# Kernel tuning notes

Measured on AMD Instinct MI355X. Metric: run time of the kernel, lower is better.

## Reference

```python
import jax, jax.numpy as jnp
import numpy as np

B, D = 32768, 64  # batch, input_dim == output_dim (k == d forced by the layer's nesting)


def setup_inputs() -> dict:
    key = jax.random.key(0)
    ks = jax.random.split(key, 9)
    f = lambda k_, sh, s=1.0: jax.random.normal(k_, sh, dtype=jnp.float32) * s
    # 0.02 / 0.1 scales keep tanh out of full saturation (init choice, not math change)
    return {
        "e1": f(ks[0], (B, D)),
        "p": f(ks[1], (B, D)),
        "e2": f(ks[2], (B, D)),
        "er": f(ks[3], (B, D)),
        "T1": f(ks[4], (D, D, D), 0.02),
        "T2": f(ks[5], (D, D, D), 0.02),
        "T3": f(ks[6], (D, D, D), 0.02),
        "W": f(ks[7], (D, 2 * D), 0.1),
        "b": jnp.zeros((D, 1), dtype=jnp.float32),
    }


def reference(e1, p, e2, er, T1, T2, T3, W, b):
    def ntn(a, c, T):
        # a, c: (B, d); T: (k, d, d) -> (k, B)
        bil = jnp.einsum("bi,kij,bj->kb", a, T, c)          # batched bilinear forms
        ff = jnp.einsum("kf,bf->kb", W, jnp.concatenate([a, c], axis=1))
        return jnp.tanh(bil + ff + b)                        # b: (k,1) broadcasts over batch

    a1 = ntn(e1, p, T1).T   # (B, k)
    c2 = ntn(p, e2, T2).T   # (B, k)  (original recomputes this for ur; identical value)
    u = ntn(a1, c2, T3)     # (k, B)
    ar = ntn(er, p, T1).T   # (B, k)
    ur = ntn(ar, c2, T3)    # (k, B)
    # concat of (B, d, 1) slabs along last axis -> (B, d, 2)
    return jnp.stack([u.T, ur.T], axis=2)
```

## Files before the change

### kernel.cpp

```cpp
#include <hip/hip_runtime.h>
#include <hip/hip_bf16.h>
#include <math.h>

#define BATCH 32768

typedef __attribute__((ext_vector_type(8))) short short8v;
typedef __attribute__((ext_vector_type(4))) float f32x4;
typedef __attribute__((ext_vector_type(2))) float f32x2;
typedef unsigned short u16;
typedef unsigned char u8;

#define MFMA16 __builtin_amdgcn_mfma_f32_16x16x32_bf16

#define TILE_AB 32768
#define TILE_C  65536
#define SMB     81920

#define WS_T(t) ((size_t)(t)*524288)
#define WS_W    1572864

static __device__ __forceinline__ u16 f2bf(float x) {
    __hip_bfloat16 h = __float2bfloat16(x);
    return *reinterpret_cast<u16*>(&h);
}
static __device__ __forceinline__ float bf2f(u16 v) {
    __hip_bfloat16 h = *reinterpret_cast<__hip_bfloat16*>(&v);
    return __bfloat162float(h);
}

__global__ void presplit_kernel(const float* __restrict__ T1, const float* __restrict__ T2,
                                const float* __restrict__ T3, const float* __restrict__ W,
                                u8* __restrict__ ws)
{
    const int idx = blockIdx.x * 256 + threadIdx.x;
    const int NT = 3 * 262144;
    if (idx < NT) {
        const int t = idx >> 18;
        const int r = idx & 262143;
        const int k = r >> 12, i = (r >> 6) & 63, j = r & 63;
        const float* Ts = (t == 0) ? T1 : (t == 1) ? T2 : T3;
        const int kt = k >> 4, klr = k & 15;
        const int pc = (j >> 3) ^ (klr & 7);
        const size_t base = WS_T(t) + (size_t)i * 8192 + kt * 2048 + klr * 128
                          + pc * 16 + (j & 7) * 2;
        *(u16*)(ws + base) = f2bf(Ts[r]);
    } else if (idx < NT + 16384) {
        const int r = idx - NT;
        const int plane = r >> 12, k = (r >> 6) & 63, j = r & 63;
        const int half = plane >> 1, lo = plane & 1;
        const float x = W[k * 128 + half * 64 + j];
        const u16 hh = f2bf(x);
        const u16 v = lo ? f2bf(x - bf2f(hh)) : hh;
        *(u16*)(ws + WS_W + (size_t)plane * 8192 + (k * 64 + j) * 2) = v;
    }
}

__device__ __forceinline__ void stage16(const void* g, void* l) {
    __builtin_amdgcn_global_load_lds((const __attribute__((address_space(1))) unsigned int*)g,
                                     (__attribute__((address_space(3))) unsigned int*)l, 16, 0, 0);
}
__device__ __forceinline__ void stage_slice(u8* sm, const u8* slice, int buf, int w, int l) {
    stage16(slice + w * 1024 + l * 16, sm + buf * 8192 + w * 1024);
}

struct Frag2 { short8v h, l; };
__device__ __forceinline__ Frag2 split8(const float* __restrict__ src) {
    Frag2 f;
#pragma unroll
    for (int e = 0; e < 8; ++e) {
        const float x = src[e];
        const u16 h = f2bf(x);
        f.h[e] = (short)h;
        f.l[e] = (short)f2bf(x - bf2f(h));
    }
    return f;
}
__device__ __forceinline__ Frag2 gather_c(const u8* sm, int b, int f0) {
    float tmp[8];
#pragma unroll
    for (int e = 0; e < 8; ++e)
        tmp[e] = *(const float*)(sm + TILE_C + (f0 + e) * 256 + b * 4);
    return split8(tmp);
}
__device__ __forceinline__ void gather_ab(const u8* sm, int b, int f0, Frag2& fa, Frag2& fb) {
    float t0[8], t1[8];
#pragma unroll
    for (int e = 0; e < 8; ++e) {
        const f32x2 v = *(const f32x2*)(sm + TILE_AB + (size_t)(f0 + e) * 512 + b * 8);
        t0[e] = v.x; t1[e] = v.y;
    }
    fa = split8(t0); fb = split8(t1);
}
__device__ __forceinline__ f32x4 mfma3(short8v Ah, short8v Al, short8v Bh, short8v Bl, f32x4 acc) {
    acc = MFMA16(Ah, Bh, acc, 0, 0, 0);
    acc = MFMA16(Ah, Bl, acc, 0, 0, 0);
    acc = MFMA16(Al, Bh, acc, 0, 0, 0);
    return acc;
}

template<int MODE>
__device__ void pass_run(u8* sm, const u8* __restrict__ ws,
                         const float* __restrict__ gC, const float* __restrict__ gA0,
                         const float* __restrict__ gA1,
                         const float* __restrict__ bias, float* __restrict__ outg,
                         int B0, int w, int kt, int jh, int l, int lr, int lq, int tid)
{
    constexpr int NV = (MODE == 1) ? 1 : 2;
    const u8* tws = ws + WS_T(MODE);

    stage_slice(sm, tws,                    0, w, l);
    stage_slice(sm, tws + (size_t)1 * 8192, 1, w, l);
    stage_slice(sm, tws + (size_t)2 * 8192, 2, w, l);

    short8v Bh[4], Bl[4];
#pragma unroll
    for (int nt = 0; nt < 4; ++nt) {
        const int b = nt * 16 + lr;
        Frag2 f;
        if (MODE < 2) f = split8(gC + (size_t)(B0 + b) * 64 + jh * 32 + lq * 8);
        else          f = gather_c(sm, b, jh * 32 + lq * 8);
        Bh[nt] = f.h; Bl[nt] = f.l;
    }

    f32x4 bil[NV][4];
    {
        const u16* Wp = (const u16*)(ws + WS_W);
        if (jh == 0) {
            short8v w2h[2], w2l[2];
#pragma unroll
            for (int h = 0; h < 2; ++h) {
                const int off = (kt * 16 + lr) * 64 + h * 32 + lq * 8;
                w2h[h] = *(const short8v*)(Wp + 8192 + off);
                w2l[h] = *(const short8v*)(Wp + 12288 + off);
            }
            const f32x4 bv4 = *(const f32x4*)(bias + kt * 16 + lq * 4);
#pragma unroll
            for (int nt = 0; nt < 4; ++nt) {
                const int b = nt * 16 + lr;
                f32x4 s = {0.f, 0.f, 0.f, 0.f};
#pragma unroll
                for (int h = 0; h < 2; ++h) {
                    Frag2 fc;
                    if (MODE < 2) fc = split8(gC + (size_t)(B0 + b) * 64 + h * 32 + lq * 8);
                    else          fc = gather_c(sm, b, h * 32 + lq * 8);
                    s = mfma3(w2h[h], w2l[h], fc.h, fc.l, s);
                }
#pragma unroll
                for (int v = 0; v < NV; ++v)
#pragma unroll
                for (int rg = 0; rg < 4; ++rg) bil[v][nt][rg] = s[rg] + bv4[rg];
            }
        } else {
            short8v w1h[2], w1l[2];
#pragma unroll
            for (int h = 0; h < 2; ++h) {
                const int off = (kt * 16 + lr) * 64 + h * 32 + lq * 8;
                w1h[h] = *(const short8v*)(Wp + off);
                w1l[h] = *(const short8v*)(Wp + 4096 + off);
            }
#pragma unroll
            for (int nt = 0; nt < 4; ++nt) {
                const int b = nt * 16 + lr;
                f32x4 sv0 = {0.f, 0.f, 0.f, 0.f};
                f32x4 sv1 = {0.f, 0.f, 0.f, 0.f};
#pragma unroll
                for (int h = 0; h < 2; ++h) {
                    Frag2 fa, fb;
                    if (MODE == 0) {
                        fa = split8(gA0 + (size_t)(B0 + b) * 64 + h * 32 + lq * 8);
                        fb = split8(gA1 + (size_t)(B0 + b) * 64 + h * 32 + lq * 8);
                    } else if (MODE == 1) {
                        fa = split8(gA0 + (size_t)(B0 + b) * 64 + h * 32 + lq * 8);
                    } else {
                        gather_ab(sm, b, h * 32 + lq * 8, fa, fb);
                    }
                    sv0 = mfma3(w1h[h], w1l[h], fa.h, fa.l, sv0);
                    if (NV == 2) sv1 = mfma3(w1h[h], w1l[h], fb.h, fb.l, sv1);
                }
                bil[0][nt] = sv0;
                if (NV == 2) bil[1][nt] = sv1;
            }
        }
    }

    const int tswz = kt * 2048 + lr * 128 + (((jh * 4 + lq) ^ (lr & 7)) << 4);
    const f32x4 ZERO4 = {0.f, 0.f, 0.f, 0.f};

#define STEP(I, VMN, DOSTG) do {                                                           \
    f32x2 sv[4];                                                                           \
    _Pragma("unroll") for (int nt = 0; nt < 4; ++nt) {                                     \
        if (MODE == 1) sv[nt].x = *(const float*)(sm + TILE_C + (I) * 256 + nt * 64 + lr * 4); \
        else sv[nt] = *(const f32x2*)(sm + TILE_AB + (I) * 512 + nt * 128 + lr * 8);       \
    }                                                                                      \
    asm volatile("s_waitcnt vmcnt(" #VMN ")" ::: "memory");                                \
    __builtin_amdgcn_sched_barrier(0);                                                     \
    __builtin_amdgcn_s_barrier();                                                          \
    __builtin_amdgcn_sched_barrier(0);                                                     \
    if (DOSTG) stage_slice(sm, tws + (size_t)((I) + 3) * 8192, ((I) + 3) & 3, w, l);       \
    const u8* tb_ = sm + ((I) & 3) * 8192 + tswz;                                          \
    const short8v Th_ = *(const short8v*)tb_;                                              \
    f32x4 S_[4];                                                                           \
    __builtin_amdgcn_s_setprio(1);                                                         \
    _Pragma("unroll") for (int nt = 0; nt < 4; ++nt) {                                     \
        f32x4 z_ = MFMA16(Th_, Bh[nt], ZERO4, 0, 0, 0);                                    \
        S_[nt] = MFMA16(Th_, Bl[nt], z_, 0, 0, 0);                                         \
    }                                                                                      \
    __builtin_amdgcn_s_setprio(0);                                                         \
    _Pragma("unroll") for (int nt = 0; nt < 4; ++nt)                                       \
    _Pragma("unroll") for (int rg = 0; rg < 4; ++rg) {                                     \
        bil[0][nt][rg] += sv[nt].x * S_[nt][rg];                                           \
        if (NV == 2) bil[1][nt][rg] += sv[nt].y * S_[nt][rg];                              \
    }                                                                                      \
} while (0)

#pragma unroll 4
    for (int i = 0; i < 60; ++i) STEP(i, 2, true);
    STEP(60, 2, true);
    STEP(61, 2, false);
    STEP(62, 1, false);
    STEP(63, 0, false);
#undef STEP

    __syncthreads();
    float* PRE = (float*)sm;
    if (jh == 1) {
#pragma unroll
        for (int v = 0; v < NV; ++v)
#pragma unroll
        for (int nt = 0; nt < 4; ++nt)
#pragma unroll
        for (int rg = 0; rg < 4; ++rg)
            PRE[v * 4096 + (kt * 16 + lq * 4 + rg) * 64 + nt * 16 + lr] = bil[v][nt][rg];
    }
    __syncthreads();

    if (MODE == 0) {
        if (jh == 0) {
#pragma unroll
            for (int nt = 0; nt < 4; ++nt) {
                const int b = nt * 16 + lr;
#pragma unroll
                for (int rg = 0; rg < 4; ++rg) {
                    const int k = kt * 16 + lq * 4 + rg;
                    f32x2 o;
                    o.x = tanhf(bil[0][nt][rg] + PRE[k * 64 + b]);
                    o.y = tanhf(bil[1][nt][rg] + PRE[4096 + k * 64 + b]);
                    *(f32x2*)(sm + TILE_AB + (size_t)k * 512 + b * 8) = o;
                }
            }
        }
        __syncthreads();
    } else if (MODE == 1) {
        if (jh == 0) {
#pragma unroll
            for (int nt = 0; nt < 4; ++nt) {
                const int b = nt * 16 + lr;
#pragma unroll
                for (int rg = 0; rg < 4; ++rg) {
                    const int k = kt * 16 + lq * 4 + rg;
                    *(float*)(sm + TILE_C + k * 256 + b * 4) =
                        tanhf(bil[0][nt][rg] + PRE[k * 64 + b]);
                }
            }
        }
        __syncthreads();
    } else {
        f32x2 ures[4][4];
        if (jh == 0) {
#pragma unroll
            for (int nt = 0; nt < 4; ++nt) {
                const int b = nt * 16 + lr;
#pragma unroll
                for (int rg = 0; rg < 4; ++rg) {
                    const int k = kt * 16 + lq * 4 + rg;
                    ures[nt][rg].x = tanhf(bil[0][nt][rg] + PRE[k * 64 + b]);
                    ures[nt][rg].y = tanhf(bil[1][nt][rg] + PRE[4096 + k * 64 + b]);
                }
            }
        }
        __syncthreads();
        if (jh == 0) {
#pragma unroll
            for (int nt = 0; nt < 4; ++nt) {
                const int b = nt * 16 + lr;
#pragma unroll
                for (int rg = 0; rg < 4; ++rg) {
                    const int k = kt * 16 + lq * 4 + rg;
                    *(f32x2*)(sm + b * 512 + (((k ^ b) & 63) << 3)) = ures[nt][rg];
                }
            }
        }
        __syncthreads();
        const int bq = tid >> 3, t = tid & 7;
        float o[16];
#pragma unroll
        for (int kk = 0; kk < 8; ++kk) {
            const int k = t * 8 + kk;
            const f32x2 pr = *(const f32x2*)(sm + bq * 512 + (((k ^ bq) & 63) << 3));
            o[kk * 2] = pr.x; o[kk * 2 + 1] = pr.y;
        }
        float* dst = outg + (size_t)(B0 + bq) * 128 + t * 16;
#pragma unroll
        for (int q = 0; q < 4; ++q) *(f32x4*)(dst + q * 4) = *(const f32x4*)(o + q * 4);
    }
}

__global__ __launch_bounds__(512, 4)
void ntn_main(const float* __restrict__ e1, const float* __restrict__ p,
              const float* __restrict__ e2, const float* __restrict__ er,
              const float* __restrict__ bias, const u8* __restrict__ ws,
              float* __restrict__ out)
{
    __shared__ __align__(16) u8 sm[SMB];
    const int tid = threadIdx.x;
    const int l = tid & 63;
    const int w = __builtin_amdgcn_readfirstlane(tid >> 6);
    const int kt = w & 3, jh = w >> 2;
    const int lr = l & 15, lq = l >> 4;
    const int B0 = blockIdx.x * 64;

    {
        const int b = tid >> 3, f0 = (tid & 7) * 8;
        const size_t g = (size_t)(B0 + b) * 64 + f0;
        const f32x4 a0 = *(const f32x4*)(e1 + g), a1v = *(const f32x4*)(e1 + g + 4);
        const f32x4 r0 = *(const f32x4*)(er + g), r1v = *(const f32x4*)(er + g + 4);
        const f32x4 p0 = *(const f32x4*)(p + g),  p1v = *(const f32x4*)(p + g + 4);
#pragma unroll
        for (int e = 0; e < 4; ++e) {
            f32x2 v0; v0.x = a0[e]; v0.y = r0[e];
            *(f32x2*)(sm + TILE_AB + (size_t)(f0 + e) * 512 + b * 8) = v0;
            f32x2 v1; v1.x = a1v[e]; v1.y = r1v[e];
            *(f32x2*)(sm + TILE_AB + (size_t)(f0 + 4 + e) * 512 + b * 8) = v1;
            *(float*)(sm + TILE_C + (f0 + e) * 256 + b * 4) = p0[e];
            *(float*)(sm + TILE_C + (f0 + 4 + e) * 256 + b * 4) = p1v[e];
        }
    }
    __syncthreads();

    pass_run<0>(sm, ws, p,  e1, er,      bias, nullptr, B0, w, kt, jh, l, lr, lq, tid);
    pass_run<1>(sm, ws, e2, p,  nullptr, bias, nullptr, B0, w, kt, jh, l, lr, lq, tid);
    pass_run<2>(sm, ws, nullptr, nullptr, nullptr, bias, out, B0, w, kt, jh, l, lr, lq, tid);
}

extern "C" void kernel_launch(void* const* d_in, const int* in_sizes, int n_in,
                              void* d_out, int out_size, void* d_ws, size_t ws_size,
                              hipStream_t stream) {
    const float* e1   = (const float*)d_in[0];
    const float* p    = (const float*)d_in[1];
    const float* e2   = (const float*)d_in[2];
    const float* er   = (const float*)d_in[3];
    const float* T1   = (const float*)d_in[4];
    const float* T2   = (const float*)d_in[5];
    const float* T3   = (const float*)d_in[6];
    const float* W    = (const float*)d_in[7];
    const float* bias = (const float*)d_in[8];

    u8* ws = (u8*)d_ws;
    hipLaunchKernelGGL(presplit_kernel, dim3(3136), dim3(256), 0, stream, T1, T2, T3, W, ws);
    hipLaunchKernelGGL(ntn_main, dim3(BATCH / 64), dim3(512), 0, stream,
                       e1, p, e2, er, bias, (const u8*)ws, (float*)d_out);
}
```

Measured before the change: 141.9 us.

## Process two T slices per barrier with double-slice staging

Restructures the slice pipeline so each iteration consumes two 8KB T slices per barrier and stages the next two, halving the number of block barriers. The prefetch depth drops from three slices in flight to two, and each barrier waits on vmcnt(0), so load latency is less hidden. This trades barrier overhead for a shallower pipeline.

After: 139.4 us, median of 2. About the same (-1.7%).

```diff
diff --git a/kernel.cpp b/kernel.cpp
--- a/kernel.cpp
+++ b/kernel.cpp
@@ -110,7 +110,6 @@
 
     stage_slice(sm, tws,                    0, w, l);
     stage_slice(sm, tws + (size_t)1 * 8192, 1, w, l);
-    stage_slice(sm, tws + (size_t)2 * 8192, 2, w, l);
 
     short8v Bh[4], Bl[4];
 #pragma unroll
@@ -186,40 +185,57 @@
     const int tswz = kt * 2048 + lr * 128 + (((jh * 4 + lq) ^ (lr & 7)) << 4);
     const f32x4 ZERO4 = {0.f, 0.f, 0.f, 0.f};
 
-#define STEP(I, VMN, DOSTG) do {                                                           \
-    f32x2 sv[4];                                                                           \
+#define STEP2(I0, DOSTG) do {                                                              \
+    f32x2 sva[4], svb[4];                                                                  \
     _Pragma("unroll") for (int nt = 0; nt < 4; ++nt) {                                     \
-        if (MODE == 1) sv[nt].x = *(const float*)(sm + TILE_C + (I) * 256 + nt * 64 + lr * 4); \
-        else sv[nt] = *(const f32x2*)(sm + TILE_AB + (I) * 512 + nt * 128 + lr * 8);       \
-    }                                                                                      \
-    asm volatile("s_waitcnt vmcnt(" #VMN ")" ::: "memory");                                \
+        if (MODE == 1) {                                                                   \
+            sva[nt].x = *(const float*)(sm + TILE_C + (I0) * 256 + nt * 64 + lr * 4);      \
+            svb[nt].x = *(const float*)(sm + TILE_C + ((I0) + 1) * 256 + nt * 64 + lr * 4);\
+        } else {                                                                           \
+            sva[nt] = *(const f32x2*)(sm + TILE_AB + (I0) * 512 + nt * 128 + lr * 8);      \
+            svb[nt] = *(const f32x2*)(sm + TILE_AB + ((I0) + 1) * 512 + nt * 128 + lr * 8);\
+        }                                                                                  \
+    }                                                                                      \
+    asm volatile("s_waitcnt vmcnt(0)" ::: "memory");                                       \
     __builtin_amdgcn_sched_barrier(0);                                                     \
     __builtin_amdgcn_s_barrier();                                                          \
     __builtin_amdgcn_sched_barrier(0);                                                     \
-    if (DOSTG) stage_slice(sm, tws + (size_t)((I) + 3) * 8192, ((I) + 3) & 3, w, l);       \
-    const u8* tb_ = sm + ((I) & 3) * 8192 + tswz;                                          \
-    const short8v Th_ = *(const short8v*)tb_;                                              \
-    f32x4 S_[4];                                                                           \
+    if (DOSTG) {                                                                           \
+        stage_slice(sm, tws + (size_t)((I0) + 2) * 8192, ((I0) + 2) & 3, w, l);            \
+        stage_slice(sm, tws + (size_t)((I0) + 3) * 8192, ((I0) + 3) & 3, w, l);            \
+    }                                                                                      \
+    const short8v Tha_ = *(const short8v*)(sm + ((I0) & 3) * 8192 + tswz);                 \
+    f32x4 Sa_[4];                                                                          \
     __builtin_amdgcn_s_setprio(1);                                                         \
     _Pragma("unroll") for (int nt = 0; nt < 4; ++nt) {                                     \
-        f32x4 z_ = MFMA16(Th_, Bh[nt], ZERO4, 0, 0, 0);                                    \
-        S_[nt] = MFMA16(Th_, Bl[nt], z_, 0, 0, 0);                                         \
+        f32x4 z_ = MFMA16(Tha_, Bh[nt], ZERO4, 0, 0, 0);                                   \
+        Sa_[nt] = MFMA16(Tha_, Bl[nt], z_, 0, 0, 0);                                       \
     }                                                                                      \
     __builtin_amdgcn_s_setprio(0);                                                         \
     _Pragma("unroll") for (int nt = 0; nt < 4; ++nt)                                       \
     _Pragma("unroll") for (int rg = 0; rg < 4; ++rg) {                                     \
-        bil[0][nt][rg] += sv[nt].x * S_[nt][rg];                                           \
-        if (NV == 2) bil[1][nt][rg] += sv[nt].y * S_[nt][rg];                              \
+        bil[0][nt][rg] += sva[nt].x * Sa_[nt][rg];                                         \
+        if (NV == 2) bil[1][nt][rg] += sva[nt].y * Sa_[nt][rg];                            \
+    }                                                                                      \
+    const short8v Thb_ = *(const short8v*)(sm + (((I0) + 1) & 3) * 8192 + tswz);           \
+    f32x4 Sb_[4];                                                                          \
+    __builtin_amdgcn_s_setprio(1);                                                         \
+    _Pragma("unroll") for (int nt = 0; nt < 4; ++nt) {                                     \
+        f32x4 z_ = MFMA16(Thb_, Bh[nt], ZERO4, 0, 0, 0);                                   \
+        Sb_[nt] = MFMA16(Thb_, Bl[nt], z_, 0, 0, 0);                                       \
+    }                                                                                      \
+    __builtin_amdgcn_s_setprio(0);                                                         \
+    _Pragma("unroll") for (int nt = 0; nt < 4; ++nt)                                       \
+    _Pragma("unroll") for (int rg = 0; rg < 4; ++rg) {                                     \
+        bil[0][nt][rg] += svb[nt].x * Sb_[nt][rg];                                         \
+        if (NV == 2) bil[1][nt][rg] += svb[nt].y * Sb_[nt][rg];                            \
     }                                                                                      \
 } while (0)
 
-#pragma unroll 4
-    for (int i = 0; i < 60; ++i) STEP(i, 2, true);
-    STEP(60, 2, true);
-    STEP(61, 2, false);
-    STEP(62, 1, false);
-    STEP(63, 0, false);
-#undef STEP
+#pragma unroll 2
+    for (int s = 0; s < 31; ++s) STEP2(s * 2, true);
+    STEP2(62, false);
+#undef STEP2
 
     __syncthreads();
     float* PRE = (float*)sm;
```
